# Optimization experiments

Measured on AMD Instinct MI355X. Metric: run time of the kernel, lower is better.

Reference implementation:

```python
import jax, jax.numpy as jnp
import numpy as np

D_MODEL = 2048
NUM_HEADS = 16
D_K = D_MODEL // NUM_HEADS  # 128
BATCH, SEQ = 2, 2048


def setup_inputs() -> dict:
    key = jax.random.key(0)
    ks = jax.random.split(key, 9)
    s = 0.02
    return {
        "x": jax.random.normal(ks[0], (BATCH, SEQ, D_MODEL), dtype=jnp.float32),
        "W_q": jax.random.normal(ks[1], (D_MODEL, D_MODEL), dtype=jnp.float32) * s,
        "b_q": jax.random.normal(ks[2], (D_MODEL,), dtype=jnp.float32) * s,
        "W_k": jax.random.normal(ks[3], (D_MODEL, D_K), dtype=jnp.float32) * s,
        "b_k": jax.random.normal(ks[4], (D_K,), dtype=jnp.float32) * s,
        "W_v": jax.random.normal(ks[5], (D_MODEL, D_K), dtype=jnp.float32) * s,
        "b_v": jax.random.normal(ks[6], (D_K,), dtype=jnp.float32) * s,
        "W_o": jax.random.normal(ks[7], (D_MODEL, D_MODEL), dtype=jnp.float32) * s,
        "b_o": jax.random.normal(ks[8], (D_MODEL,), dtype=jnp.float32) * s,
    }


def reference(x, W_q, b_q, W_k, b_k, W_v, b_v, W_o, b_o):
    B, S, _ = x.shape
    # Q: per-head projections -> (B, H, S, d_k)
    Q = (x @ W_q + b_q).reshape(B, S, NUM_HEADS, D_K).transpose(0, 2, 1, 3)
    # K, V: single shared head -> (B, S, d_k)
    K = x @ W_k + b_k
    V = x @ W_v + b_v
    scale = 1.0 / np.sqrt(D_K)
    # scores: (B, H, S_q, S_k); K broadcast across heads (no expand materialized)
    scores = jnp.einsum("bhqd,bkd->bhqk", Q, K) * scale
    attn = jax.nn.softmax(scores, axis=-1)
    out = jnp.einsum("bhqk,bkd->bhqd", attn, V)  # (B, H, S, d_k)
    out = out.transpose(0, 2, 1, 3).reshape(B, S, D_MODEL)
    out = out @ W_o + b_o
    K_cache = K[:, None, :, :]  # (B, 1, S, d_k)
    V_cache = V[:, None, :, :]
    return (out, K_cache, V_cache)
```

## Files before the change

### kernel.cpp

```cpp
#include <hip/hip_runtime.h>
#include <cstdint>

typedef __bf16 bf16x8 __attribute__((ext_vector_type(8)));
typedef short s16x4 __attribute__((ext_vector_type(4)));
typedef float f32x4 __attribute__((ext_vector_type(4)));
typedef unsigned short ushort_t;

constexpr int kS  = 2048;
constexpr int kDM = 2048;
constexpr int kDK = 128;
constexpr int kNH = 16;
constexpr int kB  = 2;
constexpr int kNQKV = kDM + 2 * kDK;

__device__ __forceinline__ unsigned short f2bf(float f) {
  union { float f; unsigned u; } v; v.f = f;
  unsigned u = v.u;
  u += 0x7fffu + ((u >> 16) & 1u);
  return (unsigned short)(u >> 16);
}

__device__ __forceinline__ void gload16(const void* g, void* l) {
  __builtin_amdgcn_global_load_lds(
      (const __attribute__((address_space(1))) void*)g,
      (__attribute__((address_space(3))) void*)l, 16, 0, 0);
}

__global__ __launch_bounds__(256) void cast_f32_bf16(const float* __restrict__ in,
                                                     ushort_t* __restrict__ out, long n) {
  long i = ((long)blockIdx.x * 256 + threadIdx.x) * 4;
  if (i >= n) return;
  float4 f = *reinterpret_cast<const float4*>(in + i);
  ushort4 o;
  o.x = f2bf(f.x); o.y = f2bf(f.y); o.z = f2bf(f.z); o.w = f2bf(f.w);
  *reinterpret_cast<ushort4*>(out + i) = o;
}

__global__ __launch_bounds__(256) void transpose_cast(const float* __restrict__ in,
                                                      ushort_t* __restrict__ out,
                                                      int R, int C) {
  __shared__ float tile[32][33];
  int c = blockIdx.x * 32 + threadIdx.x;
  int r0 = blockIdx.y * 32;
  #pragma unroll
  for (int i = threadIdx.y; i < 32; i += 8)
    tile[i][threadIdx.x] = in[(long)(r0 + i) * C + c];
  __syncthreads();
  int oc  = r0 + threadIdx.x;
  int or0 = blockIdx.x * 32;
  #pragma unroll
  for (int i = threadIdx.y; i < 32; i += 8)
    out[(long)(or0 + i) * R + oc] = f2bf(tile[threadIdx.x][i]);
}

__device__ __forceinline__ void gemm128(const ushort_t* __restrict__ A, int lda,
                                        const ushort_t* __restrict__ Bt, int ldb,
                                        int K, int row0, int col0,
                                        f32x4 (&acc)[4][4]) {
  __shared__ __align__(16) ushort_t sA[128 * 32];
  __shared__ __align__(16) ushort_t sB[128 * 32];
  int t = threadIdx.x;
  int r = t >> 2, c4 = t & 3;
  const ushort_t* gA0 = A  + (long)(row0 + r)      * lda + c4 * 8;
  const ushort_t* gA1 = A  + (long)(row0 + r + 64) * lda + c4 * 8;
  const ushort_t* gB0 = Bt + (long)(col0 + r)      * ldb + c4 * 8;
  const ushort_t* gB1 = Bt + (long)(col0 + r + 64) * ldb + c4 * 8;
  int lane = t & 63, wave = t >> 6;
  int wr = wave >> 1, wc = wave & 1;
  int lr = lane & 15, lg = lane >> 4;
  int aoff = (wr * 64 + lr) * 32 + lg * 8;
  int boff = (wc * 64 + lr) * 32 + lg * 8;

  for (int kk = 0; kk < K; kk += 32) {
    gload16(gA0 + kk, (void*)(sA + t * 8));
    gload16(gA1 + kk, (void*)(sA + 2048 + t * 8));
    gload16(gB0 + kk, (void*)(sB + t * 8));
    gload16(gB1 + kk, (void*)(sB + 2048 + t * 8));
    __syncthreads();
    bf16x8 af[4], bg[4];
    #pragma unroll
    for (int i = 0; i < 4; i++) af[i] = *(const bf16x8*)(sA + aoff + i * 16 * 32);
    #pragma unroll
    for (int j = 0; j < 4; j++) bg[j] = *(const bf16x8*)(sB + boff + j * 16 * 32);
    #pragma unroll
    for (int i = 0; i < 4; i++)
      #pragma unroll
      for (int j = 0; j < 4; j++)
        acc[i][j] = __builtin_amdgcn_mfma_f32_16x16x32_bf16(af[i], bg[j], acc[i][j], 0, 0, 0);
    __syncthreads();
  }
}

__global__ __launch_bounds__(256) void gemm_qkv(const ushort_t* __restrict__ x,
    const ushort_t* __restrict__ Wt, const float* __restrict__ bq,
    const float* __restrict__ bk, const float* __restrict__ bv,
    ushort_t* __restrict__ Qb, float* __restrict__ Kc,
    ushort_t* __restrict__ Kb, float* __restrict__ Vc, ushort_t* __restrict__ Vtb) {
  f32x4 acc[4][4] = {};
  int row0 = blockIdx.y * 128, col0 = blockIdx.x * 128;
  gemm128(x, kDM, Wt, kDM, kDM, row0, col0, acc);
  int lane = threadIdx.x & 63, wave = threadIdx.x >> 6;
  int wr = wave >> 1, wc = wave & 1, lr = lane & 15, lg = lane >> 4;
  #pragma unroll
  for (int i = 0; i < 4; i++) {
    #pragma unroll
    for (int j = 0; j < 4; j++) {
      int col = col0 + wc * 64 + j * 16 + lr;
      float bias = (col < kDM) ? bq[col]
                 : (col < kDM + kDK) ? bk[col - kDM] : bv[col - kDM - kDK];
      #pragma unroll
      for (int rr = 0; rr < 4; rr++) {
        int row = row0 + wr * 64 + i * 16 + lg * 4 + rr;
        float v = acc[i][j][rr] + bias;
        if (col < kDM) {
          Qb[(long)row * kDM + col] = f2bf(v);
        } else if (col < kDM + kDK) {
          int c = col - kDM;
          Kc[(long)row * kDK + c] = v;
          Kb[(long)row * kDK + c] = f2bf(v);
        } else {
          int c = col - kDM - kDK;
          Vc[(long)row * kDK + c] = v;
          Vtb[((long)(row >> 11) * kDK + c) * kS + (row & 2047)] = f2bf(v);
        }
      }
    }
  }
}

__global__ __launch_bounds__(256) void gemm_out(const ushort_t* __restrict__ A,
    const ushort_t* __restrict__ Wt, const float* __restrict__ bias,
    float* __restrict__ C) {
  f32x4 acc[4][4] = {};
  int row0 = blockIdx.y * 128, col0 = blockIdx.x * 128;
  gemm128(A, kDM, Wt, kDM, kDM, row0, col0, acc);
  int lane = threadIdx.x & 63, wave = threadIdx.x >> 6;
  int wr = wave >> 1, wc = wave & 1, lr = lane & 15, lg = lane >> 4;
  #pragma unroll
  for (int i = 0; i < 4; i++) {
    #pragma unroll
    for (int j = 0; j < 4; j++) {
      int col = col0 + wc * 64 + j * 16 + lr;
      float bv = bias[col];
      #pragma unroll
      for (int rr = 0; rr < 4; rr++) {
        int row = row0 + wr * 64 + i * 16 + lg * 4 + rr;
        C[(long)row * kDM + col] = acc[i][j][rr] + bv;
      }
    }
  }
}

__global__ __launch_bounds__(256, 2) void flash_attn(
    const ushort_t* __restrict__ Qb, const ushort_t* __restrict__ Kb,
    const ushort_t* __restrict__ Vt, ushort_t* __restrict__ Ob) {
  __shared__ __align__(16) ushort_t sK[128 * 128];
  __shared__ __align__(16) ushort_t sV[128 * 128];

  const int tid = threadIdx.x;
  const int L = tid & 63, wave = tid >> 6;
  const int lr = L & 15, lg = L >> 4;
  const int bh = blockIdx.y, b = bh >> 4, h = bh & 15;
  const int q0 = blockIdx.x * 128;

  const ushort_t* Kg = Kb + (long)b * kS * kDK;
  const ushort_t* Vg = Vt + (long)b * kDK * kS;
  const ushort_t* Qg = Qb + ((long)b * kS + q0 + wave * 32) * kDM + h * kDK;

  bf16x8 qf[2][4];
  #pragma unroll
  for (int i = 0; i < 2; i++)
    #pragma unroll
    for (int kk = 0; kk < 4; kk++)
      qf[i][kk] = *(const bf16x8*)(Qg + (long)(i * 16 + lr) * kDM + kk * 32 + lg * 8);

  f32x4 accO[8][2] = {};
  float lsum[2] = {};

  for (int j = 0; j < 16; j++) {
    __syncthreads();
    #pragma unroll
    for (int s = 0; s < 8; s++) {
      int c = tid + s * 256;
      int f = c >> 6, cl = c & 63;
      gload16(Kg + (long)(j * 128 + (f >> 2) * 16 + (cl & 15)) * kDK + (f & 3) * 32 + (cl >> 4) * 8,
              (void*)(sK + c * 8));
      int d = c >> 4, kb = (c & 15) ^ (d & 15);
      gload16(Vg + (long)d * kS + j * 128 + kb * 8, (void*)(sV + c * 8));
    }
    __syncthreads();

    #pragma unroll
    for (int half = 0; half < 2; half++) {
      f32x4 sacc[4][2] = {};
      #pragma unroll
      for (int kk = 0; kk < 4; kk++)
        #pragma unroll
        for (int s = 0; s < 4; s++) {
          bf16x8 kf = *(const bf16x8*)(sK + ((half * 4 + s) * 4 + kk) * 512 + L * 8);
          #pragma unroll
          for (int i = 0; i < 2; i++)
            sacc[s][i] = __builtin_amdgcn_mfma_f32_16x16x32_bf16(kf, qf[i][kk], sacc[s][i], 0, 0, 0);
        }

      s16x4 pf[4][2];
      #pragma unroll
      for (int s = 0; s < 4; s++)
        #pragma unroll
        for (int i = 0; i < 2; i++)
          #pragma unroll
          for (int r = 0; r < 4; r++) {
            float p = __expf(sacc[s][i][r] * 0.08838834764831845f);
            lsum[i] += p;
            pf[s][i][r] = (short)f2bf(p);
          }

      #pragma unroll
      for (int s = 0; s < 4; s++) {
        int ss = half * 4 + s;
        int kbL = (ss * 2 + (lg >> 1)) ^ lr;
        int voff = lr * 128 + kbL * 8 + (lg & 1) * 4;
        #pragma unroll
        for (int t = 0; t < 8; t++) {
          s16x4 vf = *(const s16x4*)(sV + t * 2048 + voff);
          #pragma unroll
          for (int i = 0; i < 2; i++)
            accO[t][i] = __builtin_amdgcn_mfma_f32_16x16x16bf16_1k(vf, pf[s][i], accO[t][i], 0, 0, 0);
        }
      }
    }
  }

  float inv[2];
  #pragma unroll
  for (int i = 0; i < 2; i++) {
    float v = lsum[i];
    v += __shfl_xor(v, 16);
    v += __shfl_xor(v, 32);
    inv[i] = 1.0f / v;
  }

  ushort_t* Og = Ob + ((long)b * kS + q0 + wave * 32) * kDM + h * kDK;
  #pragma unroll
  for (int t = 0; t < 8; t++)
    #pragma unroll
    for (int i = 0; i < 2; i++) {
      ushort4 o;
      o.x = f2bf(accO[t][i][0] * inv[i]);
      o.y = f2bf(accO[t][i][1] * inv[i]);
      o.z = f2bf(accO[t][i][2] * inv[i]);
      o.w = f2bf(accO[t][i][3] * inv[i]);
      *(ushort4*)(Og + (long)(i * 16 + lr) * kDM + t * 16 + lg * 4) = o;
    }
}

extern "C" void kernel_launch(void* const* d_in, const int* in_sizes, int n_in,
                              void* d_out, int out_size, void* d_ws, size_t ws_size,
                              hipStream_t stream) {
  (void)in_sizes; (void)n_in; (void)out_size; (void)ws_size;
  const float* x   = (const float*)d_in[0];
  const float* W_q = (const float*)d_in[1];
  const float* b_q = (const float*)d_in[2];
  const float* W_k = (const float*)d_in[3];
  const float* b_k = (const float*)d_in[4];
  const float* W_v = (const float*)d_in[5];
  const float* b_v = (const float*)d_in[6];
  const float* W_o = (const float*)d_in[7];
  const float* b_o = (const float*)d_in[8];

  float* out = (float*)d_out;
  float* Kc  = out + (long)kB * kS * kDM;
  float* Vc  = Kc  + (long)kB * kS * kDK;

  char* w = (char*)d_ws;
  ushort_t* x_bf   = (ushort_t*)w;  w += 16777216;
  ushort_t* Wall_t = (ushort_t*)w;  w += (size_t)kNQKV*kDM*2;
  ushort_t* Wo_t   = (ushort_t*)w;  w += 8388608;
  ushort_t* Q_bf   = (ushort_t*)w;  w += 16777216;
  ushort_t* K_bf   = (ushort_t*)w;  w += 1048576;
  ushort_t* Vt_bf  = (ushort_t*)w;  w += 1048576;
  ushort_t* O_bf   = (ushort_t*)w;  w += 16777216;

  dim3 blk(256);
  dim3 tblk(32, 8);

  cast_f32_bf16<<<dim3(8192), blk, 0, stream>>>(x, x_bf, (long)kB * kS * kDM);
  transpose_cast<<<dim3(64, 64), tblk, 0, stream>>>(W_q, Wall_t, kDM, kDM);
  transpose_cast<<<dim3(4, 64),  tblk, 0, stream>>>(W_k, Wall_t + (long)kDM * kDM, kDM, kDK);
  transpose_cast<<<dim3(4, 64),  tblk, 0, stream>>>(W_v, Wall_t + (long)(kDM + kDK) * kDM, kDM, kDK);
  transpose_cast<<<dim3(64, 64), tblk, 0, stream>>>(W_o, Wo_t, kDM, kDM);

  gemm_qkv<<<dim3(kNQKV / 128, kB * kS / 128), blk, 0, stream>>>(
      x_bf, Wall_t, b_q, b_k, b_v, Q_bf, Kc, K_bf, Vc, Vt_bf);

  flash_attn<<<dim3(kS / 128, kB * kNH), blk, 0, stream>>>(Q_bf, K_bf, Vt_bf, O_bf);

  gemm_out<<<dim3(kDM / 128, kB * kS / 128), blk, 0, stream>>>(O_bf, Wo_t, b_o, out);
}
```

Measured before the change: 339.0 us.

## Use 16x16x32 MFMA for PV via permuted K layout, exp2 and packed bf16 cvt

Permutes the key order in the K shared-memory load so the score accumulators of two 16-key tiles form one 32-key bf16x8 operand. This lets the PV product use the wider 16x16x32 MFMA with 8-element V fragments instead of twice as many 16x16x16 MFMAs with 4-element fragments. It also replaces __expf with exp2 and a prescaled log2e constant, swaps the software bf16 rounding for the hardware v_cvt_pk_bf16_f32 instruction, and adds s_setprio hints around the MFMA phases. The key permutation must match the V swizzle exactly, so any indexing mismatch would silently produce wrong results.

```diff
diff --git a/kernel.cpp b/kernel.cpp
--- a/kernel.cpp
+++ b/kernel.cpp
@@ -2,7 +2,6 @@
 #include <cstdint>
 
 typedef __bf16 bf16x8 __attribute__((ext_vector_type(8)));
-typedef short s16x4 __attribute__((ext_vector_type(4)));
 typedef float f32x4 __attribute__((ext_vector_type(4)));
 typedef unsigned short ushort_t;
 
@@ -177,13 +176,17 @@
   f32x4 accO[8][2] = {};
   float lsum[2] = {};
 
+  constexpr float kScaleLog2e = 0.12751743f;
+
   for (int j = 0; j < 16; j++) {
     __syncthreads();
     #pragma unroll
-    for (int s = 0; s < 8; s++) {
-      int c = tid + s * 256;
+    for (int s8 = 0; s8 < 8; s8++) {
+      int c = tid + s8 * 256;
       int f = c >> 6, cl = c & 63;
-      gload16(Kg + (long)(j * 128 + (f >> 2) * 16 + (cl & 15)) * kDK + (f & 3) * 32 + (cl >> 4) * 8,
+      int st = f >> 2, kk = f & 3, n = cl & 15;
+      int key = (st >> 1) * 32 + (n >> 2) * 8 + (st & 1) * 4 + (n & 3);
+      gload16(Kg + (long)(j * 128 + key) * kDK + kk * 32 + (cl >> 4) * 8,
               (void*)(sK + c * 8));
       int d = c >> 4, kb = (c & 15) ^ (d & 15);
       gload16(Vg + (long)d * kS + j * 128 + kb * 8, (void*)(sV + c * 8));
@@ -191,43 +194,47 @@
     __syncthreads();
 
     #pragma unroll
-    for (int half = 0; half < 2; half++) {
-      f32x4 sacc[4][2] = {};
+    for (int u = 0; u < 4; u++) {
+      f32x4 sacc[2][2] = {};
+      __builtin_amdgcn_s_setprio(1);
       #pragma unroll
       for (int kk = 0; kk < 4; kk++)
         #pragma unroll
-        for (int s = 0; s < 4; s++) {
-          bf16x8 kf = *(const bf16x8*)(sK + ((half * 4 + s) * 4 + kk) * 512 + L * 8);
+        for (int jj = 0; jj < 2; jj++) {
+          bf16x8 kf = *(const bf16x8*)(sK + ((u * 2 + jj) * 4 + kk) * 512 + L * 8);
           #pragma unroll
           for (int i = 0; i < 2; i++)
-            sacc[s][i] = __builtin_amdgcn_mfma_f32_16x16x32_bf16(kf, qf[i][kk], sacc[s][i], 0, 0, 0);
+            sacc[jj][i] = __builtin_amdgcn_mfma_f32_16x16x32_bf16(kf, qf[i][kk], sacc[jj][i], 0, 0, 0);
         }
-
-      s16x4 pf[4][2];
-      #pragma unroll
-      for (int s = 0; s < 4; s++)
+      __builtin_amdgcn_s_setprio(0);
+
+      bf16x8 pf[2];
+      #pragma unroll
+      for (int i = 0; i < 2; i++) {
+        union { bf16x8 v; unsigned w[4]; } P;
+        #pragma unroll
+        for (int jj = 0; jj < 2; jj++) {
+          float p0 = __builtin_amdgcn_exp2f(sacc[jj][i][0] * kScaleLog2e);
+          float p1 = __builtin_amdgcn_exp2f(sacc[jj][i][1] * kScaleLog2e);
+          float p2 = __builtin_amdgcn_exp2f(sacc[jj][i][2] * kScaleLog2e);
+          float p3 = __builtin_amdgcn_exp2f(sacc[jj][i][3] * kScaleLog2e);
+          lsum[i] += (p0 + p1) + (p2 + p3);
+          asm("v_cvt_pk_bf16_f32 %0, %1, %2" : "=v"(P.w[jj * 2 + 0]) : "v"(p0), "v"(p1));
+          asm("v_cvt_pk_bf16_f32 %0, %1, %2" : "=v"(P.w[jj * 2 + 1]) : "v"(p2), "v"(p3));
+        }
+        pf[i] = P.v;
+      }
+
+      __builtin_amdgcn_s_setprio(1);
+      #pragma unroll
+      for (int t = 0; t < 8; t++) {
+        int kbL = (u * 4 + lg) ^ lr;
+        bf16x8 vf = *(const bf16x8*)(sV + t * 2048 + lr * 128 + kbL * 8);
         #pragma unroll
         for (int i = 0; i < 2; i++)
-          #pragma unroll
-          for (int r = 0; r < 4; r++) {
-            float p = __expf(sacc[s][i][r] * 0.08838834764831845f);
-            lsum[i] += p;
-            pf[s][i][r] = (short)f2bf(p);
-          }
-
-      #pragma unroll
-      for (int s = 0; s < 4; s++) {
-        int ss = half * 4 + s;
-        int kbL = (ss * 2 + (lg >> 1)) ^ lr;
-        int voff = lr * 128 + kbL * 8 + (lg & 1) * 4;
-        #pragma unroll
-        for (int t = 0; t < 8; t++) {
-          s16x4 vf = *(const s16x4*)(sV + t * 2048 + voff);
-          #pragma unroll
-          for (int i = 0; i < 2; i++)
-            accO[t][i] = __builtin_amdgcn_mfma_f32_16x16x16bf16_1k(vf, pf[s][i], accO[t][i], 0, 0, 0);
-        }
+          accO[t][i] = __builtin_amdgcn_mfma_f32_16x16x32_bf16(vf, pf[i], accO[t][i], 0, 0, 0);
       }
+      __builtin_amdgcn_s_setprio(0);
     }
   }
 
@@ -245,12 +252,14 @@
   for (int t = 0; t < 8; t++)
     #pragma unroll
     for (int i = 0; i < 2; i++) {
-      ushort4 o;
-      o.x = f2bf(accO[t][i][0] * inv[i]);
-      o.y = f2bf(accO[t][i][1] * inv[i]);
-      o.z = f2bf(accO[t][i][2] * inv[i]);
-      o.w = f2bf(accO[t][i][3] * inv[i]);
-      *(ushort4*)(Og + (long)(i * 16 + lr) * kDM + t * 16 + lg * 4) = o;
+      union { ushort4 o; unsigned w[2]; } O;
+      float f0 = accO[t][i][0] * inv[i];
+      float f1 = accO[t][i][1] * inv[i];
+      float f2 = accO[t][i][2] * inv[i];
+      float f3 = accO[t][i][3] * inv[i];
+      asm("v_cvt_pk_bf16_f32 %0, %1, %2" : "=v"(O.w[0]) : "v"(f0), "v"(f1));
+      asm("v_cvt_pk_bf16_f32 %0, %1, %2" : "=v"(O.w[1]) : "v"(f2), "v"(f3));
+      *(ushort4*)(Og + (long)(i * 16 + lr) * kDM + t * 16 + lg * 4) = O.o;
     }
 }
 
```

Measured after the change: 317.2 us. 6.4% less time.
